# Optimization experiments

Measured on AMD Instinct MI355X. Metric: run time of the kernel, lower is better.

The kernel has to match this reference:

```python
import jax, jax.numpy as jnp
import numpy as np

EPS = 1e-08
RMAX = 8.0          # hist_range_max
BINS = 256
ALPHA = 0.02        # kalman_alpha (EMA rate)
THRESH = -2.0       # mask_threshold


def setup_inputs() -> dict:
    key = jax.random.key(0)
    B, C, L = 4, 5, 2097152
    x = jax.random.normal(key, (B, C, L), dtype=jnp.float32)
    # running histogram buffer, initialized to ones as in the module
    hist = jnp.ones((C, BINS), dtype=jnp.float32)
    # analytic reference log-pdfs over the bin grid
    grid = jnp.linspace(EPS, RMAX, BINS)
    logp_ref = jnp.stack([
        jnp.log(grid) - 0.5 * grid ** 2,                 # Rayleigh-like (A)
        -1.5 * jnp.log1p((grid / (RMAX / 2)) ** 2),      # heavy-tail (theta')
        -grid,                                            # exponential (A^2)
        -0.5 * grid ** 2,                                 # half-gaussian (AA')
        -0.5 * grid ** 2,                                 # half-gaussian (A^2 theta')
    ], axis=0) + EPS
    return {"x": x, "hist": hist, "logp_ref": logp_ref.astype(jnp.float32)}


def reference(x, hist, logp_ref):
    B, C, L = x.shape
    # NOTE: torch does x.reshape(C, -1) on a (B, C, L) tensor, i.e. a raw
    # memory reinterpretation (no permute). Replicate exactly.
    flat_abs = jnp.abs(x.reshape(C, B * L))                     # (C, B*L)
    # per-channel 99th-percentile normalization (linear interpolation, like torch)
    max_vals = jnp.maximum(
        jnp.quantile(flat_abs, 0.99, axis=-1, keepdims=True), EPS)
    normalized = flat_abs / max_vals * RMAX
    clipped = jnp.clip(normalized, 0.0, RMAX - EPS)
    idx = (clipped / RMAX * (BINS - 1)).astype(jnp.int32)       # floor (nonneg)
    idx = jnp.clip(idx, 0, BINS - 1)                            # (C, B*L)

    # histogram scatter-add per channel (vectorized over all channels)
    ch = jnp.broadcast_to(jnp.arange(C)[:, None], idx.shape)
    new_hist = jnp.zeros((C, BINS), dtype=x.dtype).at[ch, idx].add(1.0)

    # EMA update of the running histogram
    hist = (1.0 - ALPHA) * hist + ALPHA * new_hist
    smoothed = hist + EPS
    logp_obs = jnp.log(smoothed / jnp.sum(smoothed, axis=-1, keepdims=True))

    # gather per-sample log-probs and form the log-likelihood ratio
    logp_ref_s = jnp.take_along_axis(logp_ref, idx, axis=-1)   # (C, B*L)
    logp_obs_s = jnp.take_along_axis(logp_obs, idx, axis=-1)   # (C, B*L)
    Lam = (logp_ref_s - logp_obs_s).reshape(B, C, L)

    mask = jax.nn.sigmoid(-(Lam - THRESH))   # beta = 1.0
    return x * mask
```

## Files before the change

kernel.cpp:

```cpp
#include <hip/hip_runtime.h>
#include <math.h>

typedef unsigned int u32;
typedef unsigned long long u64;
typedef long long i64;

#define BINS 256
#define TBITS 0x40000000u
#define A_BASE 131072u
#define A_BINS 4096
#define B_BINS 8192
#define SLOT 1536
#define NBLK 512


__device__ __forceinline__ int bin_index_f32(float xv, float mv) {
    float r = __fdiv_rn(fabsf(xv), mv);
    r = fminf(r, 1.0f);
    return (int)__fmul_rn(r, 255.0f);
}

template<int PER>
__device__ void block_select(const u32* __restrict__ h, u32 target,
                             u32* ssum, u32* res) {
    const int t = threadIdx.x;
    u32 loc[PER];
    u32 s = 0;
    const int base = t * PER;
#pragma unroll
    for (int j = 0; j < PER; ++j) { loc[j] = h[base + j]; s += loc[j]; }
    ssum[t] = s;
    __syncthreads();
    for (int off = 1; off < 256; off <<= 1) {
        u32 add = (t >= off) ? ssum[t - off] : 0;
        __syncthreads();
        ssum[t] += add;
        __syncthreads();
    }
    u32 cum = ssum[t] - s;
#pragma unroll
    for (int j = 0; j < PER; ++j) {
        u32 cnt = loc[j];
        if (target >= cum && target < cum + cnt) { res[0] = (u32)(base + j); res[1] = target - cum; }
        cum += cnt;
    }
    __syncthreads();
}

__device__ __forceinline__ float np_lerp_f32(u32 v0bits, u32 v1bits, double gamma) {
    float v0 = __uint_as_float(v0bits);
    float v1 = __uint_as_float(v1bits);
    float dba = __fsub_rn(v1, v0);
    float q;
    if (gamma >= 0.5) q = __fsub_rn(v1, __fmul_rn(dba, (float)(1.0 - gamma)));
    else              q = __fadd_rn(v0, __fmul_rn(dba, (float)gamma));
    return fmaxf(q, 1e-8f);
}


__global__ __launch_bounds__(256) void k_pass1(const float* __restrict__ x, u32* __restrict__ cand,
                                               u32* __restrict__ gha, u32* __restrict__ oflow,
                                               u32* __restrict__ goob, i64 nper, int do_cand) {
    __shared__ u32 lbuf[SLOT];
    __shared__ u32 lha[A_BINS];
    __shared__ u32 lcnt, loob;
    const int c = blockIdx.y;
    for (int i = threadIdx.x; i < A_BINS; i += 256) lha[i] = 0;
    if (threadIdx.x == 0) { lcnt = 0; loob = 0; }
    __syncthreads();
    const float* xc = x + (i64)c * nper;
    const i64 nv2 = nper >> 3;
    const float4* xv = (const float4*)xc;
    for (i64 i = (i64)blockIdx.x * 256 + threadIdx.x; i < nv2; i += (i64)gridDim.x * 256) {
        float4 a = xv[2 * i], b = xv[2 * i + 1];
        u32 bb[8];
        bb[0] = __float_as_uint(fabsf(a.x)); bb[1] = __float_as_uint(fabsf(a.y));
        bb[2] = __float_as_uint(fabsf(a.z)); bb[3] = __float_as_uint(fabsf(a.w));
        bb[4] = __float_as_uint(fabsf(b.x)); bb[5] = __float_as_uint(fabsf(b.y));
        bb[6] = __float_as_uint(fabsf(b.z)); bb[7] = __float_as_uint(fabsf(b.w));
#pragma unroll
        for (int k = 0; k < 8; ++k) {
            if (bb[k] >= TBITS) {
                u32 p = atomicAdd(&lcnt, 1u);
                if (p < SLOT) lbuf[p] = bb[k];
                u32 bin = (bb[k] >> 13) - A_BASE;
                if (bin >= A_BINS) { atomicAdd(&loob, 1u); bin = A_BINS - 1; }
                atomicAdd(&lha[bin], 1u);
            }
        }
    }
    if (blockIdx.x == 0 && threadIdx.x < (int)(nper & 7)) {
        u32 b = __float_as_uint(fabsf(xc[nv2 * 8 + threadIdx.x]));
        if (b >= TBITS) {
            u32 p = atomicAdd(&lcnt, 1u);
            if (p < SLOT) lbuf[p] = b;
            u32 bin = (b >> 13) - A_BASE;
            if (bin >= A_BINS) { atomicAdd(&loob, 1u); bin = A_BINS - 1; }
            atomicAdd(&lha[bin], 1u);
        }
    }
    __syncthreads();
    for (int i = threadIdx.x; i < A_BINS; i += 256)
        if (lha[i]) atomicAdd(&gha[c * A_BINS + i], lha[i]);
    if (threadIdx.x == 0) {
        if (loob) atomicExch(&goob[c], 1u);
        if (lcnt > SLOT) { atomicExch(&oflow[c], 1u); lcnt = SLOT; }
    }
    __syncthreads();
    if (do_cand) {
        const u32 cnt = lcnt;
        u32* slot = cand + ((i64)c * gridDim.x + blockIdx.x) * SLOT;
        for (u32 j = threadIdx.x; j < SLOT; j += 256)
            slot[j] = (j < cnt) ? lbuf[j] : 0u;
    }
}


__global__ __launch_bounds__(256) void k_cselA_pick(const u32* __restrict__ gha,
                                                    const u32* __restrict__ oflow, const u32* __restrict__ goob,
                                                    u32* __restrict__ flag, u32* __restrict__ cselA, u32 needed) {
    __shared__ u32 ssum[256];
    __shared__ u32 pr[4];
    __shared__ u32 s_total;
    const int c = blockIdx.x;
    const int t = threadIdx.x;
    if (t < 4) pr[t] = 0;
    const u32* h = gha + c * A_BINS;
    u32 loc[16];
    u32 s = 0;
    const int base = t * 16;
#pragma unroll
    for (int j = 0; j < 16; ++j) { loc[j] = h[base + j]; s += loc[j]; }
    ssum[t] = s;
    __syncthreads();
    for (int off = 1; off < 256; off <<= 1) {
        u32 add = (t >= off) ? ssum[t - off] : 0;
        __syncthreads();
        ssum[t] += add;
        __syncthreads();
    }
    if (t == 255) s_total = ssum[255];
    __syncthreads();
    const u32 total = s_total;
    const u32 bad = (oflow[c] != 0) || (goob[c] != 0) || (total < needed) || (needed < 2);
    if (t == 0) flag[c] = bad;
    if (bad) return;
    const u32 t0 = total - needed;
    const u32 t1 = t0 + 1;
    u32 cum = ssum[t] - s;
#pragma unroll
    for (int j = 0; j < 16; ++j) {
        u32 cnt = loc[j];
        if (t0 >= cum && t0 < cum + cnt) { pr[0] = (u32)(base + j); pr[1] = t0 - cum; }
        if (t1 >= cum && t1 < cum + cnt) { pr[2] = (u32)(base + j); pr[3] = t1 - cum; }
        cum += cnt;
    }
    __syncthreads();
    if (t == 0) {
        cselA[c * 4 + 0] = pr[0]; cselA[c * 4 + 1] = pr[1];
        cselA[c * 4 + 2] = pr[2]; cselA[c * 4 + 3] = pr[3];
    }
}


__global__ __launch_bounds__(256) void k_cselB_hist(const u32* __restrict__ cand, const u32* __restrict__ flag,
                                                    const u32* __restrict__ cselA,
                                                    u32* __restrict__ g3a, u32* __restrict__ g3b, i64 ntot) {
    const int c = blockIdx.y;
    if (flag[c]) return;
    __shared__ u32 la[B_BINS], lb[B_BINS];
    for (int i = threadIdx.x; i < B_BINS; i += 256) { la[i] = 0; lb[i] = 0; }
    __syncthreads();
    const u32 topA0 = A_BASE + cselA[c * 4 + 0];
    const u32 topA1 = A_BASE + cselA[c * 4 + 2];
    const uint4* cd = (const uint4*)(cand + (i64)c * ntot);
    const i64 nv4 = ntot >> 2;
    for (i64 i = (i64)blockIdx.x * 256 + threadIdx.x; i < nv4; i += (i64)gridDim.x * 256) {
        uint4 v = cd[i];
        u32 b;
        b = v.x;
        if (b >= TBITS) { u32 tb = b >> 13; if (tb == topA0) atomicAdd(&la[b & (B_BINS - 1)], 1u); if (tb == topA1) atomicAdd(&lb[b & (B_BINS - 1)], 1u); }
        b = v.y;
        if (b >= TBITS) { u32 tb = b >> 13; if (tb == topA0) atomicAdd(&la[b & (B_BINS - 1)], 1u); if (tb == topA1) atomicAdd(&lb[b & (B_BINS - 1)], 1u); }
        b = v.z;
        if (b >= TBITS) { u32 tb = b >> 13; if (tb == topA0) atomicAdd(&la[b & (B_BINS - 1)], 1u); if (tb == topA1) atomicAdd(&lb[b & (B_BINS - 1)], 1u); }
        b = v.w;
        if (b >= TBITS) { u32 tb = b >> 13; if (tb == topA0) atomicAdd(&la[b & (B_BINS - 1)], 1u); if (tb == topA1) atomicAdd(&lb[b & (B_BINS - 1)], 1u); }
    }
    __syncthreads();
    for (int i = threadIdx.x; i < B_BINS; i += 256) {
        if (la[i]) atomicAdd(&g3a[c * B_BINS + i], la[i]);
        if (lb[i]) atomicAdd(&g3b[c * B_BINS + i], lb[i]);
    }
}

__global__ __launch_bounds__(256) void k_cselB_pick(const u32* __restrict__ g3a, const u32* __restrict__ g3b,
                                                    const u32* __restrict__ flag, const u32* __restrict__ cselA,
                                                    float* __restrict__ mv, double gamma) {
    __shared__ u32 ssum[256];
    __shared__ u32 pr[4];
    const int c = blockIdx.x;
    if (flag[c]) return;
    if (threadIdx.x < 4) pr[threadIdx.x] = 0;
    __syncthreads();
    block_select<32>(g3a + c * B_BINS, cselA[c * 4 + 1], ssum, &pr[0]);
    block_select<32>(g3b + c * B_BINS, cselA[c * 4 + 3], ssum, &pr[2]);
    if (threadIdx.x == 0) {
        u32 v0bits = ((A_BASE + cselA[c * 4 + 0]) << 13) | pr[0];
        u32 v1bits = ((A_BASE + cselA[c * 4 + 2]) << 13) | pr[2];
        mv[c] = np_lerp_f32(v0bits, v1bits, gamma);
    }
}

__global__ void k_flag_force(u32* __restrict__ flag, int C) {
    if (threadIdx.x < C) flag[threadIdx.x] = 1u;
}


__global__ __launch_bounds__(256) void k_fallback(const float* __restrict__ x, const u32* __restrict__ flag,
                                                  float* __restrict__ mv, i64 nper, u32 k0, double gamma) {
    const int c = blockIdx.x;
    if (!flag[c]) return;
    __shared__ u32 h0[2048], h1[2048];
    __shared__ u32 ssum[256];
    __shared__ u32 pr[4];
    __shared__ u32 st[4];
    const float* xc = x + (i64)c * nper;
    const i64 nv = nper >> 2;
    const int rem = (int)(nper & 3);
    const float4* xv = (const float4*)xc;
    const int t = threadIdx.x;

    for (int i = t; i < 1024; i += 256) h0[i] = 0;
    __syncthreads();
    for (i64 i = t; i < nv; i += 256) {
        float4 v = xv[i];
        atomicAdd(&h0[__float_as_uint(fabsf(v.x)) >> 21], 1u);
        atomicAdd(&h0[__float_as_uint(fabsf(v.y)) >> 21], 1u);
        atomicAdd(&h0[__float_as_uint(fabsf(v.z)) >> 21], 1u);
        atomicAdd(&h0[__float_as_uint(fabsf(v.w)) >> 21], 1u);
    }
    if (t < rem) atomicAdd(&h0[__float_as_uint(fabsf(xc[nv * 4 + t])) >> 21], 1u);
    __syncthreads();
    if (t < 4) pr[t] = 0;
    __syncthreads();
    block_select<4>(h0, k0, ssum, &pr[0]);
    block_select<4>(h0, k0 + 1, ssum, &pr[2]);
    if (t < 4) st[t] = pr[t];
    __syncthreads();

    const u32 p0 = st[0], p1 = st[2];
    for (int i = t; i < 2048; i += 256) { h0[i] = 0; h1[i] = 0; }
    __syncthreads();
    for (i64 i = t; i < nv; i += 256) {
        float4 v = xv[i];
        u32 b;
        b = __float_as_uint(fabsf(v.x));
        if ((b >> 21) == p0) atomicAdd(&h0[(b >> 10) & 2047], 1u);
        if ((b >> 21) == p1) atomicAdd(&h1[(b >> 10) & 2047], 1u);
        b = __float_as_uint(fabsf(v.y));
        if ((b >> 21) == p0) atomicAdd(&h0[(b >> 10) & 2047], 1u);
        if ((b >> 21) == p1) atomicAdd(&h1[(b >> 10) & 2047], 1u);
        b = __float_as_uint(fabsf(v.z));
        if ((b >> 21) == p0) atomicAdd(&h0[(b >> 10) & 2047], 1u);
        if ((b >> 21) == p1) atomicAdd(&h1[(b >> 10) & 2047], 1u);
        b = __float_as_uint(fabsf(v.w));
        if ((b >> 21) == p0) atomicAdd(&h0[(b >> 10) & 2047], 1u);
        if ((b >> 21) == p1) atomicAdd(&h1[(b >> 10) & 2047], 1u);
    }
    if (t < rem) {
        u32 b = __float_as_uint(fabsf(xc[nv * 4 + t]));
        if ((b >> 21) == p0) atomicAdd(&h0[(b >> 10) & 2047], 1u);
        if ((b >> 21) == p1) atomicAdd(&h1[(b >> 10) & 2047], 1u);
    }
    __syncthreads();
    if (t < 4) pr[t] = 0;
    __syncthreads();
    block_select<8>(h0, st[1], ssum, &pr[0]);
    block_select<8>(h1, st[3], ssum, &pr[2]);
    if (t == 0) { st[0] = (p0 << 11) | pr[0]; st[1] = pr[1]; st[2] = (p1 << 11) | pr[2]; st[3] = pr[3]; }
    __syncthreads();

    const u32 q0 = st[0], q1 = st[2];
    for (int i = t; i < 1024; i += 256) { h0[i] = 0; h1[i] = 0; }
    __syncthreads();
    for (i64 i = t; i < nv; i += 256) {
        float4 v = xv[i];
        u32 b;
        b = __float_as_uint(fabsf(v.x));
        if ((b >> 10) == q0) atomicAdd(&h0[b & 1023], 1u);
        if ((b >> 10) == q1) atomicAdd(&h1[b & 1023], 1u);
        b = __float_as_uint(fabsf(v.y));
        if ((b >> 10) == q0) atomicAdd(&h0[b & 1023], 1u);
        if ((b >> 10) == q1) atomicAdd(&h1[b & 1023], 1u);
        b = __float_as_uint(fabsf(v.z));
        if ((b >> 10) == q0) atomicAdd(&h0[b & 1023], 1u);
        if ((b >> 10) == q1) atomicAdd(&h1[b & 1023], 1u);
        b = __float_as_uint(fabsf(v.w));
        if ((b >> 10) == q0) atomicAdd(&h0[b & 1023], 1u);
        if ((b >> 10) == q1) atomicAdd(&h1[b & 1023], 1u);
    }
    if (t < rem) {
        u32 b = __float_as_uint(fabsf(xc[nv * 4 + t]));
        if ((b >> 10) == q0) atomicAdd(&h0[b & 1023], 1u);
        if ((b >> 10) == q1) atomicAdd(&h1[b & 1023], 1u);
    }
    __syncthreads();
    if (t < 4) pr[t] = 0;
    __syncthreads();
    block_select<4>(h0, st[1], ssum, &pr[0]);
    block_select<4>(h1, st[3], ssum, &pr[2]);
    if (t == 0) {
        u32 v0bits = (q0 << 10) | pr[0];
        u32 v1bits = (q1 << 10) | pr[2];
        mv[c] = np_lerp_f32(v0bits, v1bits, gamma);
    }
}


__global__ __launch_bounds__(256) void k_hist_idx(const float* __restrict__ x, const float* __restrict__ mv,
                                                  u32* __restrict__ h256, i64 nper) {
    __shared__ u32 lh[8][257];
    const int c = blockIdx.y;
    const float m = mv[c];
    for (int i = threadIdx.x; i < 8 * 257; i += 256) (&lh[0][0])[i] = 0;
    __syncthreads();
    const float* xc = x + (i64)c * nper;
    const i64 nv2 = nper >> 3;
    const int copy = threadIdx.x & 7;
    const float4* xv = (const float4*)xc;
    for (i64 i = (i64)blockIdx.x * 256 + threadIdx.x; i < nv2; i += (i64)gridDim.x * 256) {
        float4 a = xv[2 * i], b = xv[2 * i + 1];
        atomicAdd(&lh[copy][bin_index_f32(a.x, m)], 1u);
        atomicAdd(&lh[copy][bin_index_f32(a.y, m)], 1u);
        atomicAdd(&lh[copy][bin_index_f32(a.z, m)], 1u);
        atomicAdd(&lh[copy][bin_index_f32(a.w, m)], 1u);
        atomicAdd(&lh[copy][bin_index_f32(b.x, m)], 1u);
        atomicAdd(&lh[copy][bin_index_f32(b.y, m)], 1u);
        atomicAdd(&lh[copy][bin_index_f32(b.z, m)], 1u);
        atomicAdd(&lh[copy][bin_index_f32(b.w, m)], 1u);
    }
    if (blockIdx.x == 0 && threadIdx.x < (int)(nper & 7)) {
        atomicAdd(&lh[copy][bin_index_f32(xc[nv2 * 8 + threadIdx.x], m)], 1u);
    }
    __syncthreads();
    for (int i = threadIdx.x; i < BINS; i += 256) {
        u32 s = 0;
#pragma unroll
        for (int k = 0; k < 8; ++k) s += lh[k][i];
        if (s) atomicAdd(&h256[c * BINS + i], s);
    }
}


__global__ __launch_bounds__(256) void k_output(const float* __restrict__ x, const float* __restrict__ mv,
                                                const float* __restrict__ hist_in, const float* __restrict__ logp_ref,
                                                const u32* __restrict__ h256, float* __restrict__ out, i64 nper) {
    __shared__ double smv_s[BINS];
    __shared__ double maskl[BINS];
    __shared__ double stot;
    const int c = blockIdx.y;
    const int b = threadIdx.x;
    float h = hist_in[c * BINS + b];
    float nn = (float)h256[c * BINS + b];
    float t = __fadd_rn(__fmul_rn(0.98f, h), __fmul_rn(0.02f, nn));
    float smf = __fadd_rn(t, 1e-8f);
    double sm = (double)smf;
    smv_s[b] = sm;
    __syncthreads();
    if (b < 64) {
        double s = smv_s[b] + smv_s[b + 64] + smv_s[b + 128] + smv_s[b + 192];
        for (int o = 32; o; o >>= 1) s += __shfl_down(s, o);
        if (b == 0) stot = s;
    }
    __syncthreads();
    double Lam = (double)logp_ref[c * BINS + b] - log(sm / stot);
    maskl[b] = 1.0 / (1.0 + exp(Lam + 2.0));
    __syncthreads();

    const float m = mv[c];
    const float* xc = x + (i64)c * nper;
    float* oc = out + (i64)c * nper;
    const i64 nv2 = nper >> 3;
    const float4* xv = (const float4*)xc;
    float4* ov = (float4*)oc;
    for (i64 i = (i64)blockIdx.x * 256 + threadIdx.x; i < nv2; i += (i64)gridDim.x * 256) {
        float4 a = xv[2 * i], bb = xv[2 * i + 1];
        float4 oa, ob;
        oa.x = (float)((double)a.x * maskl[bin_index_f32(a.x, m)]);
        oa.y = (float)((double)a.y * maskl[bin_index_f32(a.y, m)]);
        oa.z = (float)((double)a.z * maskl[bin_index_f32(a.z, m)]);
        oa.w = (float)((double)a.w * maskl[bin_index_f32(a.w, m)]);
        ob.x = (float)((double)bb.x * maskl[bin_index_f32(bb.x, m)]);
        ob.y = (float)((double)bb.y * maskl[bin_index_f32(bb.y, m)]);
        ob.z = (float)((double)bb.z * maskl[bin_index_f32(bb.z, m)]);
        ob.w = (float)((double)bb.w * maskl[bin_index_f32(bb.w, m)]);
        ov[2 * i] = oa;
        ov[2 * i + 1] = ob;
    }
    if (blockIdx.x == 0 && threadIdx.x < (int)(nper & 7)) {
        i64 i = nv2 * 8 + threadIdx.x;
        float v = xc[i];
        oc[i] = (float)((double)v * maskl[bin_index_f32(v, m)]);
    }
}


extern "C" void kernel_launch(void* const* d_in, const int* in_sizes, int n_in,
                              void* d_out, int out_size, void* d_ws, size_t ws_size,
                              hipStream_t stream) {
    const float* x        = (const float*)d_in[0];
    const float* hist_in  = (const float*)d_in[1];
    const float* logp_ref = (const float*)d_in[2];
    float* out = (float*)d_out;

    const int C = in_sizes[1] / BINS;
    const i64 total = (i64)in_sizes[0];
    const i64 nper = total / C;

    char* w = (char*)d_ws;
    size_t off = 0;
    float*  mv   = (float*)(w + off);  off += 4 * ((C + 7) & ~7);
    u32* h256   = (u32*)(w + off); off += 4 * BINS * C;
    u32* oflow  = (u32*)(w + off); off += 4 * C;
    u32* goob   = (u32*)(w + off); off += 4 * C;
    u32* flag   = (u32*)(w + off); off += 4 * C;
    u32* cselA  = (u32*)(w + off); off += 4 * 4 * C;
    u32* gha    = (u32*)(w + off); off += 4 * A_BINS * C;
    u32* g3a    = (u32*)(w + off); off += 4 * B_BINS * C;
    u32* g3b    = (u32*)(w + off); off += 4 * B_BINS * C;
    const size_t zbytes = off;
    off = (off + 255) & ~(size_t)255;
    u32* cand = (u32*)(w + off);
    const i64 ntot = (i64)NBLK * SLOT;
    const size_t cand_bytes = (size_t)4 * (size_t)C * (size_t)ntot;
    const int do_cand = (ws_size >= off + cand_bytes) ? 1 : 0;

    hipMemsetAsync(d_ws, 0, zbytes, stream);

    const double virt = 0.99 * (double)(nper - 1);
    const i64 k0 = (i64)floor(virt);
    const double gamma = virt - (double)k0;
    const u32 needed = (u32)(nper - k0);

    dim3 blk(256);
    dim3 grd(NBLK, (unsigned)C);
    dim3 grd64(64, (unsigned)C);

    k_pass1<<<grd, blk, 0, stream>>>(x, cand, gha, oflow, goob, nper, do_cand);
    if (do_cand) {
        k_cselA_pick<<<(unsigned)C, blk, 0, stream>>>(gha, oflow, goob, flag, cselA, needed);
        k_cselB_hist<<<grd64, blk, 0, stream>>>(cand, flag, cselA, g3a, g3b, ntot);
        k_cselB_pick<<<(unsigned)C, blk, 0, stream>>>(g3a, g3b, flag, cselA, mv, gamma);
    } else {
        k_flag_force<<<1, 64, 0, stream>>>(flag, C);
    }
    k_fallback<<<(unsigned)C, blk, 0, stream>>>(x, flag, mv, nper, (u32)k0, gamma);
    k_hist_idx<<<grd, blk, 0, stream>>>(x, mv, h256, nper);
    k_output<<<grd, blk, 0, stream>>>(x, mv, hist_in, logp_ref, h256, out, nper);
}
```

Before: 194.9 us.

## Fuse quantile-select kernels, shrink candidate slots, use float4 loads and nontemporal stores

Merges the coarse-bin pick into the candidate histogram kernel by having every block redo the prefix scan, and folds the fine pick into the fallback kernel. This drops two small launches and the serial dependencies between them. It also shrinks the per-block candidate slot from 1536 to 1152, which cuts candidate buffer traffic but raises the chance of overflowing into the slow fallback path. The streaming loops now load one float4 per thread per iteration instead of two, and output stores are nontemporal.

```diff
diff --git a/kernel.cpp b/kernel.cpp
--- a/kernel.cpp
+++ b/kernel.cpp
@@ -4,13 +4,14 @@
 typedef unsigned int u32;
 typedef unsigned long long u64;
 typedef long long i64;
+typedef float float4n __attribute__((ext_vector_type(4)));
 
 #define BINS 256
 #define TBITS 0x40000000u
 #define A_BASE 131072u
 #define A_BINS 4096
 #define B_BINS 8192
-#define SLOT 1536
+#define SLOT 1152
 #define NBLK 512
 
 
@@ -69,35 +70,33 @@
     if (threadIdx.x == 0) { lcnt = 0; loob = 0; }
     __syncthreads();
     const float* xc = x + (i64)c * nper;
-    const i64 nv2 = nper >> 3;
+    const i64 nv = nper >> 2;
     const float4* xv = (const float4*)xc;
-    for (i64 i = (i64)blockIdx.x * 256 + threadIdx.x; i < nv2; i += (i64)gridDim.x * 256) {
-        float4 a = xv[2 * i], b = xv[2 * i + 1];
-        u32 bb[8];
-        bb[0] = __float_as_uint(fabsf(a.x)); bb[1] = __float_as_uint(fabsf(a.y));
-        bb[2] = __float_as_uint(fabsf(a.z)); bb[3] = __float_as_uint(fabsf(a.w));
-        bb[4] = __float_as_uint(fabsf(b.x)); bb[5] = __float_as_uint(fabsf(b.y));
-        bb[6] = __float_as_uint(fabsf(b.z)); bb[7] = __float_as_uint(fabsf(b.w));
-#pragma unroll
-        for (int k = 0; k < 8; ++k) {
-            if (bb[k] >= TBITS) {
-                u32 p = atomicAdd(&lcnt, 1u);
-                if (p < SLOT) lbuf[p] = bb[k];
-                u32 bin = (bb[k] >> 13) - A_BASE;
-                if (bin >= A_BINS) { atomicAdd(&loob, 1u); bin = A_BINS - 1; }
-                atomicAdd(&lha[bin], 1u);
-            }
-        }
-    }
-    if (blockIdx.x == 0 && threadIdx.x < (int)(nper & 7)) {
-        u32 b = __float_as_uint(fabsf(xc[nv2 * 8 + threadIdx.x]));
-        if (b >= TBITS) {
-            u32 p = atomicAdd(&lcnt, 1u);
-            if (p < SLOT) lbuf[p] = b;
-            u32 bin = (b >> 13) - A_BASE;
-            if (bin >= A_BINS) { atomicAdd(&loob, 1u); bin = A_BINS - 1; }
-            atomicAdd(&lha[bin], 1u);
-        }
+    for (i64 i = (i64)blockIdx.x * 256 + threadIdx.x; i < nv; i += (i64)gridDim.x * 256) {
+        float4 v = xv[i];
+        u32 b;
+        b = __float_as_uint(fabsf(v.x));
+        if (b >= TBITS) { u32 p = atomicAdd(&lcnt, 1u); if (p < SLOT) lbuf[p] = b;
+                          u32 bin = (b >> 13) - A_BASE; if (bin >= A_BINS) { atomicAdd(&loob, 1u); bin = A_BINS - 1; }
+                          atomicAdd(&lha[bin], 1u); }
+        b = __float_as_uint(fabsf(v.y));
+        if (b >= TBITS) { u32 p = atomicAdd(&lcnt, 1u); if (p < SLOT) lbuf[p] = b;
+                          u32 bin = (b >> 13) - A_BASE; if (bin >= A_BINS) { atomicAdd(&loob, 1u); bin = A_BINS - 1; }
+                          atomicAdd(&lha[bin], 1u); }
+        b = __float_as_uint(fabsf(v.z));
+        if (b >= TBITS) { u32 p = atomicAdd(&lcnt, 1u); if (p < SLOT) lbuf[p] = b;
+                          u32 bin = (b >> 13) - A_BASE; if (bin >= A_BINS) { atomicAdd(&loob, 1u); bin = A_BINS - 1; }
+                          atomicAdd(&lha[bin], 1u); }
+        b = __float_as_uint(fabsf(v.w));
+        if (b >= TBITS) { u32 p = atomicAdd(&lcnt, 1u); if (p < SLOT) lbuf[p] = b;
+                          u32 bin = (b >> 13) - A_BASE; if (bin >= A_BINS) { atomicAdd(&loob, 1u); bin = A_BINS - 1; }
+                          atomicAdd(&lha[bin], 1u); }
+    }
+    if (blockIdx.x == 0 && threadIdx.x < (int)(nper & 3)) {
+        u32 b = __float_as_uint(fabsf(xc[nv * 4 + threadIdx.x]));
+        if (b >= TBITS) { u32 p = atomicAdd(&lcnt, 1u); if (p < SLOT) lbuf[p] = b;
+                          u32 bin = (b >> 13) - A_BASE; if (bin >= A_BINS) { atomicAdd(&loob, 1u); bin = A_BINS - 1; }
+                          atomicAdd(&lha[bin], 1u); }
     }
     __syncthreads();
     for (int i = threadIdx.x; i < A_BINS; i += 256)
@@ -116,15 +115,18 @@
 }
 
 
-__global__ __launch_bounds__(256) void k_cselA_pick(const u32* __restrict__ gha,
+__global__ __launch_bounds__(256) void k_cselB_hist(const u32* __restrict__ cand, const u32* __restrict__ gha,
                                                     const u32* __restrict__ oflow, const u32* __restrict__ goob,
-                                                    u32* __restrict__ flag, u32* __restrict__ cselA, u32 needed) {
+                                                    u32* __restrict__ flag, u32* __restrict__ cselA,
+                                                    u32* __restrict__ g3a, u32* __restrict__ g3b,
+                                                    i64 ntot, u32 needed) {
+    __shared__ u32 la[B_BINS], lb[B_BINS];
     __shared__ u32 ssum[256];
-    __shared__ u32 pr[4];
+    __shared__ u32 prA[4];
     __shared__ u32 s_total;
-    const int c = blockIdx.x;
+    const int c = blockIdx.y;
     const int t = threadIdx.x;
-    if (t < 4) pr[t] = 0;
+    if (t < 4) prA[t] = 0;
     const u32* h = gha + c * A_BINS;
     u32 loc[16];
     u32 s = 0;
@@ -143,39 +145,33 @@
     __syncthreads();
     const u32 total = s_total;
     const u32 bad = (oflow[c] != 0) || (goob[c] != 0) || (total < needed) || (needed < 2);
-    if (t == 0) flag[c] = bad;
-    if (bad) return;
+    if (bad) {
+        if (blockIdx.x == 0 && t == 0) flag[c] = 1u;
+        return;
+    }
     const u32 t0 = total - needed;
     const u32 t1 = t0 + 1;
     u32 cum = ssum[t] - s;
 #pragma unroll
     for (int j = 0; j < 16; ++j) {
         u32 cnt = loc[j];
-        if (t0 >= cum && t0 < cum + cnt) { pr[0] = (u32)(base + j); pr[1] = t0 - cum; }
-        if (t1 >= cum && t1 < cum + cnt) { pr[2] = (u32)(base + j); pr[3] = t1 - cum; }
+        if (t0 >= cum && t0 < cum + cnt) { prA[0] = (u32)(base + j); prA[1] = t0 - cum; }
+        if (t1 >= cum && t1 < cum + cnt) { prA[2] = (u32)(base + j); prA[3] = t1 - cum; }
         cum += cnt;
     }
     __syncthreads();
-    if (t == 0) {
-        cselA[c * 4 + 0] = pr[0]; cselA[c * 4 + 1] = pr[1];
-        cselA[c * 4 + 2] = pr[2]; cselA[c * 4 + 3] = pr[3];
-    }
-}
-
-
-__global__ __launch_bounds__(256) void k_cselB_hist(const u32* __restrict__ cand, const u32* __restrict__ flag,
-                                                    const u32* __restrict__ cselA,
-                                                    u32* __restrict__ g3a, u32* __restrict__ g3b, i64 ntot) {
-    const int c = blockIdx.y;
-    if (flag[c]) return;
-    __shared__ u32 la[B_BINS], lb[B_BINS];
-    for (int i = threadIdx.x; i < B_BINS; i += 256) { la[i] = 0; lb[i] = 0; }
-    __syncthreads();
-    const u32 topA0 = A_BASE + cselA[c * 4 + 0];
-    const u32 topA1 = A_BASE + cselA[c * 4 + 2];
+    const u32 topA0 = A_BASE + prA[0];
+    const u32 topA1 = A_BASE + prA[2];
+    if (blockIdx.x == 0 && t == 0) {
+        flag[c] = 0u;
+        cselA[c * 4 + 0] = prA[0]; cselA[c * 4 + 1] = prA[1];
+        cselA[c * 4 + 2] = prA[2]; cselA[c * 4 + 3] = prA[3];
+    }
+    for (int i = t; i < B_BINS; i += 256) { la[i] = 0; lb[i] = 0; }
+    __syncthreads();
     const uint4* cd = (const uint4*)(cand + (i64)c * ntot);
     const i64 nv4 = ntot >> 2;
-    for (i64 i = (i64)blockIdx.x * 256 + threadIdx.x; i < nv4; i += (i64)gridDim.x * 256) {
+    for (i64 i = (i64)blockIdx.x * 256 + t; i < nv4; i += (i64)gridDim.x * 256) {
         uint4 v = cd[i];
         u32 b;
         b = v.x;
@@ -188,48 +184,45 @@
         if (b >= TBITS) { u32 tb = b >> 13; if (tb == topA0) atomicAdd(&la[b & (B_BINS - 1)], 1u); if (tb == topA1) atomicAdd(&lb[b & (B_BINS - 1)], 1u); }
     }
     __syncthreads();
-    for (int i = threadIdx.x; i < B_BINS; i += 256) {
+    for (int i = t; i < B_BINS; i += 256) {
         if (la[i]) atomicAdd(&g3a[c * B_BINS + i], la[i]);
         if (lb[i]) atomicAdd(&g3b[c * B_BINS + i], lb[i]);
     }
 }
 
-__global__ __launch_bounds__(256) void k_cselB_pick(const u32* __restrict__ g3a, const u32* __restrict__ g3b,
-                                                    const u32* __restrict__ flag, const u32* __restrict__ cselA,
-                                                    float* __restrict__ mv, double gamma) {
-    __shared__ u32 ssum[256];
-    __shared__ u32 pr[4];
-    const int c = blockIdx.x;
-    if (flag[c]) return;
-    if (threadIdx.x < 4) pr[threadIdx.x] = 0;
-    __syncthreads();
-    block_select<32>(g3a + c * B_BINS, cselA[c * 4 + 1], ssum, &pr[0]);
-    block_select<32>(g3b + c * B_BINS, cselA[c * 4 + 3], ssum, &pr[2]);
-    if (threadIdx.x == 0) {
-        u32 v0bits = ((A_BASE + cselA[c * 4 + 0]) << 13) | pr[0];
-        u32 v1bits = ((A_BASE + cselA[c * 4 + 2]) << 13) | pr[2];
-        mv[c] = np_lerp_f32(v0bits, v1bits, gamma);
-    }
-}
-
 __global__ void k_flag_force(u32* __restrict__ flag, int C) {
     if (threadIdx.x < C) flag[threadIdx.x] = 1u;
 }
 
 
-__global__ __launch_bounds__(256) void k_fallback(const float* __restrict__ x, const u32* __restrict__ flag,
+__global__ __launch_bounds__(256) void k_mv_final(const float* __restrict__ x, const u32* __restrict__ flag,
+                                                  const u32* __restrict__ cselA,
+                                                  const u32* __restrict__ g3a, const u32* __restrict__ g3b,
                                                   float* __restrict__ mv, i64 nper, u32 k0, double gamma) {
-    const int c = blockIdx.x;
-    if (!flag[c]) return;
     __shared__ u32 h0[2048], h1[2048];
     __shared__ u32 ssum[256];
     __shared__ u32 pr[4];
     __shared__ u32 st[4];
+    const int c = blockIdx.x;
+    const int t = threadIdx.x;
+
+    if (!flag[c]) {
+        if (t < 4) pr[t] = 0;
+        __syncthreads();
+        block_select<32>(g3a + c * B_BINS, cselA[c * 4 + 1], ssum, &pr[0]);
+        block_select<32>(g3b + c * B_BINS, cselA[c * 4 + 3], ssum, &pr[2]);
+        if (t == 0) {
+            u32 v0bits = ((A_BASE + cselA[c * 4 + 0]) << 13) | pr[0];
+            u32 v1bits = ((A_BASE + cselA[c * 4 + 2]) << 13) | pr[2];
+            mv[c] = np_lerp_f32(v0bits, v1bits, gamma);
+        }
+        return;
+    }
+
     const float* xc = x + (i64)c * nper;
     const i64 nv = nper >> 2;
     const int rem = (int)(nper & 3);
     const float4* xv = (const float4*)xc;
-    const int t = threadIdx.x;
 
     for (int i = t; i < 1024; i += 256) h0[i] = 0;
     __syncthreads();
@@ -326,22 +319,18 @@
     for (int i = threadIdx.x; i < 8 * 257; i += 256) (&lh[0][0])[i] = 0;
     __syncthreads();
     const float* xc = x + (i64)c * nper;
-    const i64 nv2 = nper >> 3;
+    const i64 nv = nper >> 2;
     const int copy = threadIdx.x & 7;
     const float4* xv = (const float4*)xc;
-    for (i64 i = (i64)blockIdx.x * 256 + threadIdx.x; i < nv2; i += (i64)gridDim.x * 256) {
-        float4 a = xv[2 * i], b = xv[2 * i + 1];
-        atomicAdd(&lh[copy][bin_index_f32(a.x, m)], 1u);
-        atomicAdd(&lh[copy][bin_index_f32(a.y, m)], 1u);
-        atomicAdd(&lh[copy][bin_index_f32(a.z, m)], 1u);
-        atomicAdd(&lh[copy][bin_index_f32(a.w, m)], 1u);
-        atomicAdd(&lh[copy][bin_index_f32(b.x, m)], 1u);
-        atomicAdd(&lh[copy][bin_index_f32(b.y, m)], 1u);
-        atomicAdd(&lh[copy][bin_index_f32(b.z, m)], 1u);
-        atomicAdd(&lh[copy][bin_index_f32(b.w, m)], 1u);
-    }
-    if (blockIdx.x == 0 && threadIdx.x < (int)(nper & 7)) {
-        atomicAdd(&lh[copy][bin_index_f32(xc[nv2 * 8 + threadIdx.x], m)], 1u);
+    for (i64 i = (i64)blockIdx.x * 256 + threadIdx.x; i < nv; i += (i64)gridDim.x * 256) {
+        float4 v = xv[i];
+        atomicAdd(&lh[copy][bin_index_f32(v.x, m)], 1u);
+        atomicAdd(&lh[copy][bin_index_f32(v.y, m)], 1u);
+        atomicAdd(&lh[copy][bin_index_f32(v.z, m)], 1u);
+        atomicAdd(&lh[copy][bin_index_f32(v.w, m)], 1u);
+    }
+    if (blockIdx.x == 0 && threadIdx.x < (int)(nper & 3)) {
+        atomicAdd(&lh[copy][bin_index_f32(xc[nv * 4 + threadIdx.x], m)], 1u);
     }
     __syncthreads();
     for (int i = threadIdx.x; i < BINS; i += 256) {
@@ -381,25 +370,20 @@
     const float m = mv[c];
     const float* xc = x + (i64)c * nper;
     float* oc = out + (i64)c * nper;
-    const i64 nv2 = nper >> 3;
+    const i64 nv = nper >> 2;
     const float4* xv = (const float4*)xc;
-    float4* ov = (float4*)oc;
-    for (i64 i = (i64)blockIdx.x * 256 + threadIdx.x; i < nv2; i += (i64)gridDim.x * 256) {
-        float4 a = xv[2 * i], bb = xv[2 * i + 1];
-        float4 oa, ob;
-        oa.x = (float)((double)a.x * maskl[bin_index_f32(a.x, m)]);
-        oa.y = (float)((double)a.y * maskl[bin_index_f32(a.y, m)]);
-        oa.z = (float)((double)a.z * maskl[bin_index_f32(a.z, m)]);
-        oa.w = (float)((double)a.w * maskl[bin_index_f32(a.w, m)]);
-        ob.x = (float)((double)bb.x * maskl[bin_index_f32(bb.x, m)]);
-        ob.y = (float)((double)bb.y * maskl[bin_index_f32(bb.y, m)]);
-        ob.z = (float)((double)bb.z * maskl[bin_index_f32(bb.z, m)]);
-        ob.w = (float)((double)bb.w * maskl[bin_index_f32(bb.w, m)]);
-        ov[2 * i] = oa;
-        ov[2 * i + 1] = ob;
-    }
-    if (blockIdx.x == 0 && threadIdx.x < (int)(nper & 7)) {
-        i64 i = nv2 * 8 + threadIdx.x;
+    float4n* ov = (float4n*)oc;
+    for (i64 i = (i64)blockIdx.x * 256 + threadIdx.x; i < nv; i += (i64)gridDim.x * 256) {
+        float4 v = xv[i];
+        float4n o;
+        o.x = (float)((double)v.x * maskl[bin_index_f32(v.x, m)]);
+        o.y = (float)((double)v.y * maskl[bin_index_f32(v.y, m)]);
+        o.z = (float)((double)v.z * maskl[bin_index_f32(v.z, m)]);
+        o.w = (float)((double)v.w * maskl[bin_index_f32(v.w, m)]);
+        __builtin_nontemporal_store(o, &ov[i]);
+    }
+    if (blockIdx.x == 0 && threadIdx.x < (int)(nper & 3)) {
+        i64 i = nv * 4 + threadIdx.x;
         float v = xc[i];
         oc[i] = (float)((double)v * maskl[bin_index_f32(v, m)]);
     }
@@ -420,7 +404,7 @@
 
     char* w = (char*)d_ws;
     size_t off = 0;
-    float*  mv   = (float*)(w + off);  off += 4 * ((C + 7) & ~7);
+    float* mv   = (float*)(w + off); off += 4 * ((C + 7) & ~7);
     u32* h256   = (u32*)(w + off); off += 4 * BINS * C;
     u32* oflow  = (u32*)(w + off); off += 4 * C;
     u32* goob   = (u32*)(w + off); off += 4 * C;
@@ -436,7 +420,7 @@
     const size_t cand_bytes = (size_t)4 * (size_t)C * (size_t)ntot;
     const int do_cand = (ws_size >= off + cand_bytes) ? 1 : 0;
 
-    hipMemsetAsync(d_ws, 0, zbytes, stream);
+    (void)hipMemsetAsync(d_ws, 0, zbytes, stream);
 
     const double virt = 0.99 * (double)(nper - 1);
     const i64 k0 = (i64)floor(virt);
@@ -449,13 +433,11 @@
 
     k_pass1<<<grd, blk, 0, stream>>>(x, cand, gha, oflow, goob, nper, do_cand);
     if (do_cand) {
-        k_cselA_pick<<<(unsigned)C, blk, 0, stream>>>(gha, oflow, goob, flag, cselA, needed);
-        k_cselB_hist<<<grd64, blk, 0, stream>>>(cand, flag, cselA, g3a, g3b, ntot);
-        k_cselB_pick<<<(unsigned)C, blk, 0, stream>>>(g3a, g3b, flag, cselA, mv, gamma);
+        k_cselB_hist<<<grd64, blk, 0, stream>>>(cand, gha, oflow, goob, flag, cselA, g3a, g3b, ntot, needed);
     } else {
         k_flag_force<<<1, 64, 0, stream>>>(flag, C);
     }
-    k_fallback<<<(unsigned)C, blk, 0, stream>>>(x, flag, mv, nper, (u32)k0, gamma);
+    k_mv_final<<<(unsigned)C, blk, 0, stream>>>(x, flag, cselA, g3a, g3b, mv, nper, (u32)k0, gamma);
     k_hist_idx<<<grd, blk, 0, stream>>>(x, mv, h256, nper);
     k_output<<<grd, blk, 0, stream>>>(x, mv, hist_in, logp_ref, h256, out, nper);
 }
```

New measurement: 190.5 us. -2.2%, faster.
